# Kernel tuning notes

Measured on AMD Instinct MI355X. Metric: run time of the kernel, lower is better.

The kernel has to match this reference:

```python
import jax, jax.numpy as jnp
import numpy as np

B, L, D_MODEL = 8, 256, 256
D_STATE, D_INNER, DT_RANK, D_CONV = 16, 512, 16, 4


def _ln(x, g, b, eps):
    mu = x.mean(-1, keepdims=True)
    var = ((x - mu) ** 2).mean(-1, keepdims=True)
    return (x - mu) * jax.lax.rsqrt(var + eps) * g + b


def _ssm(x, W_in, conv_w, conv_b, W_x, W_dt, b_dt, A_log, Dp, W_out):
    # x: (B, L, D_MODEL) -- standard Mamba selective-scan block
    xz = x @ W_in                                  # (B,L,2*Di)
    xc, z = jnp.split(xz, 2, axis=-1)
    K = conv_w.shape[-1]
    xp = jnp.pad(xc, ((0, 0), (K - 1, 0), (0, 0)))  # causal depthwise conv
    xc = sum(xp[:, k:k + L, :] * conv_w[:, k] for k in range(K)) + conv_b
    xc = jax.nn.silu(xc)
    x_dbl = xc @ W_x                               # (B,L,R+2S)
    dt, Bm, Cm = jnp.split(x_dbl, [DT_RANK, DT_RANK + D_STATE], axis=-1)
    dt = jax.nn.softplus(dt @ W_dt + b_dt)         # (B,L,Di)
    A = -jnp.exp(A_log)                            # (Di,S)
    dA = jnp.exp(dt[..., None] * A)                # (B,L,Di,S)
    dBx = dt[..., None] * Bm[:, :, None, :] * xc[..., None]

    def step(h, inp):
        dA_t, dBx_t, C_t = inp
        h = dA_t * h + dBx_t                       # (B,Di,S)
        y = jnp.einsum('bds,bs->bd', h, C_t)
        return h, y

    h0 = jnp.zeros((xc.shape[0], D_INNER, D_STATE), xc.dtype)
    xs = (dA.transpose(1, 0, 2, 3), dBx.transpose(1, 0, 2, 3), Cm.transpose(1, 0, 2))
    _, ys = jax.lax.scan(step, h0, xs)             # (L,B,Di)
    y = ys.transpose(1, 0, 2) + xc * Dp
    y = y * jax.nn.silu(z)
    return y @ W_out


def _basic(x, ln_g, ln_b, ssm_params):
    # Basic_Block: ReLU(SSM(LN(x))) + x  (drop_path=0, attn_drop=0)
    return jax.nn.relu(_ssm(_ln(x, ln_g, ln_b, 1e-6), *ssm_params)) + x


def setup_inputs() -> dict:
    key = jax.random.key(0)
    ks = jax.random.split(key, 32)

    def n(k, shape, s=0.02):
        return jax.random.normal(k, shape, dtype=jnp.float32) * s

    inp = {}
    inp['x_spa'] = jax.random.normal(ks[0], (B, L, D_MODEL), dtype=jnp.float32)
    inp['x_spe'] = jax.random.normal(ks[1], (B, L, D_MODEL), dtype=jnp.float32)
    i = 2
    A_init = jnp.log(jnp.tile(jnp.arange(1, D_STATE + 1, dtype=jnp.float32), (D_INNER, 1)))
    for p in ('spa', 'spe'):
        inp[p + '_ln_g'] = jnp.ones((D_MODEL,), jnp.float32)
        inp[p + '_ln_b'] = jnp.zeros((D_MODEL,), jnp.float32)
        inp[p + '_W_in'] = n(ks[i], (D_MODEL, 2 * D_INNER)); i += 1
        inp[p + '_conv_w'] = n(ks[i], (D_INNER, D_CONV), 0.1); i += 1
        inp[p + '_conv_b'] = jnp.zeros((D_INNER,), jnp.float32)
        inp[p + '_W_x'] = n(ks[i], (D_INNER, DT_RANK + 2 * D_STATE)); i += 1
        inp[p + '_W_dt'] = n(ks[i], (DT_RANK, D_INNER), 0.1); i += 1
        inp[p + '_b_dt'] = n(ks[i], (D_INNER,), 0.1); i += 1
        inp[p + '_A_log'] = A_init
        inp[p + '_D'] = jnp.ones((D_INNER,), jnp.float32)
        inp[p + '_W_out'] = n(ks[i], (D_INNER, D_MODEL)); i += 1
    inp['sc_W'] = n(ks[i], (D_MODEL, D_MODEL)); i += 1
    inp['sc_b'] = jnp.zeros((D_MODEL,), jnp.float32)
    inp['sc_ln_g'] = jnp.ones((D_MODEL,), jnp.float32)
    inp['sc_ln_b'] = jnp.zeros((D_MODEL,), jnp.float32)
    inp['fusion_W'] = n(ks[i], (D_MODEL, D_MODEL))
    return inp


def reference(x_spa, x_spe,
              spa_ln_g, spa_ln_b, spa_W_in, spa_conv_w, spa_conv_b, spa_W_x,
              spa_W_dt, spa_b_dt, spa_A_log, spa_D, spa_W_out,
              spe_ln_g, spe_ln_b, spe_W_in, spe_conv_w, spe_conv_b, spe_W_x,
              spe_W_dt, spe_b_dt, spe_A_log, spe_D, spe_W_out,
              sc_W, sc_b, sc_ln_g, sc_ln_b, fusion_W):
    # shared shortcut: Linear + LayerNorm (eps=1e-5)
    ident_spa = _ln(x_spa @ sc_W + sc_b, sc_ln_g, sc_ln_b, 1e-5)
    ident_spe = _ln(x_spe @ sc_W + sc_b, sc_ln_g, sc_ln_b, 1e-5)
    spa_p = (spa_W_in, spa_conv_w, spa_conv_b, spa_W_x, spa_W_dt, spa_b_dt, spa_A_log, spa_D, spa_W_out)
    spe_p = (spe_W_in, spe_conv_w, spe_conv_b, spe_W_x, spe_W_dt, spe_b_dt, spe_A_log, spe_D, spe_W_out)
    a = _basic(x_spa, spa_ln_g, spa_ln_b, spa_p)
    e = _basic(x_spe, spe_ln_g, spe_ln_b, spe_p)
    # fusion gate: mean-pool both branches, Linear(no bias) + sigmoid, broadcast-mul
    fw = jax.nn.sigmoid(((a.mean(1) + e.mean(1)) * 0.5) @ fusion_W)[:, None, :]
    a = a * fw
    e = e * fw
    return (a + ident_spa, e + ident_spe)
```

## Files before the change

### kernel.cpp

```cpp
#include <hip/hip_runtime.h>
#include <hip/hip_bf16.h>
#include <math.h>

#define BD 8
#define LD 256
#define DM 256
#define DS 16
#define DI 512
#define RK 16

#define NROWS (2*BD*LD)
#define HALF_ROWS (BD*LD)

typedef __attribute__((ext_vector_type(8))) short bhalf8;
typedef __attribute__((ext_vector_type(4))) float f32x4;

__device__ __forceinline__ float siluf(float x){ return x / (1.f + __expf(-x)); }
__device__ __forceinline__ float softplusf(float x){
  return fmaxf(x, 0.f) + log1pf(__expf(-fabsf(x)));
}
__device__ __forceinline__ unsigned short f2bf(float f){
  __hip_bfloat16 h = __float2bfloat16(f);
  return *reinterpret_cast<unsigned short*>(&h);
}

__global__ __launch_bounds__(256) void k_prep(
    const float* __restrict__ Wi_spa, const float* __restrict__ Wi_spe,
    const float* __restrict__ Wo_spa, const float* __restrict__ Wo_spe,
    const float* __restrict__ scW,
    const float* __restrict__ Wx_spa, const float* __restrict__ Wx_spe,
    const float* __restrict__ x_spa, const float* __restrict__ x_spe,
    const float* __restrict__ g_spa, const float* __restrict__ b_spa,
    const float* __restrict__ g_spe, const float* __restrict__ b_spe,
    unsigned short* __restrict__ Wt_i_spa, unsigned short* __restrict__ Wt_i_spe,
    unsigned short* __restrict__ Wt_o_spa, unsigned short* __restrict__ Wt_o_spe,
    unsigned short* __restrict__ scWt,
    unsigned short* __restrict__ Wxt_spa, unsigned short* __restrict__ Wxt_spe,
    unsigned short* __restrict__ xnbf, unsigned short* __restrict__ xbf,
    float* __restrict__ pooled)
{
  __shared__ __align__(16) unsigned char smem[59904];
  int b = blockIdx.x;
  int tid = threadIdx.x;
  if (b == 60){
    for (int i=tid; i<BD*DM; i+=256) pooled[i] = 0.f;
    return;
  }
  if (b >= 61){
    float (*xst)[260] = (float (*)[260])smem;
    float (*red)[16]  = (float (*)[16])(smem + 16640);
    float *mu = (float*)(smem + 17664);
    float *rs = (float*)(smem + 17728);
    int r0g = (b - 61) * 16;
    int branch = r0g >= HALF_ROWS;
    const float* xb = branch ? x_spe : x_spa;
    const float* g  = branch ? g_spe : g_spa;
    const float* be = branch ? b_spe : b_spa;
    int rr0 = branch ? r0g - HALF_ROWS : r0g;
    for (int p=0;p<4;p++){
      int i4 = tid + 256*p;
      int r = i4 >> 6, c4 = (i4 & 63)*4;
      *(float4*)&xst[r][c4] = *(const float4*)(xb + (rr0+r)*DM + c4);
    }
    __syncthreads();
    {
      int row = tid >> 4, seg = tid & 15;
      float s = 0.f, s2 = 0.f;
      #pragma unroll
      for (int i=0;i<4;i++){
        float4 v = *(float4*)&xst[row][seg*16 + i*4];
        s  += v.x+v.y+v.z+v.w;
        s2 += v.x*v.x + v.y*v.y + v.z*v.z + v.w*v.w;
      }
      red[row][seg] = s;
      __syncthreads();
      if (seg == 0){
        float t=0.f;
        #pragma unroll
        for (int i=0;i<16;i++) t += red[row][i];
        mu[row] = t * (1.f/DM);
      }
      __syncthreads();
      red[row][seg] = s2;
      __syncthreads();
      if (seg == 0){
        float t=0.f;
        #pragma unroll
        for (int i=0;i<16;i++) t += red[row][i];
        float m = mu[row];
        rs[row] = rsqrtf(t*(1.f/DM) - m*m + 1e-6f);
      }
    }
    __syncthreads();
    for (int p=0;p<4;p++){
      int i4 = tid + 256*p;
      int r = i4 >> 6, c4 = (i4 & 63)*4;
      float4 v  = *(float4*)&xst[r][c4];
      float4 gv = *(const float4*)(g + c4);
      float4 bv = *(const float4*)(be + c4);
      float m = mu[r], rv = rs[r];
      unsigned int rlo = (unsigned int)f2bf(v.x) | ((unsigned int)f2bf(v.y) << 16);
      unsigned int rhi = (unsigned int)f2bf(v.z) | ((unsigned int)f2bf(v.w) << 16);
      *(uint2*)&xbf[(r0g+r)*DM + c4] = make_uint2(rlo, rhi);
      unsigned int nlo = (unsigned int)f2bf((v.x-m)*rv*gv.x + bv.x)
                       | ((unsigned int)f2bf((v.y-m)*rv*gv.y + bv.y) << 16);
      unsigned int nhi = (unsigned int)f2bf((v.z-m)*rv*gv.z + bv.z)
                       | ((unsigned int)f2bf((v.w-m)*rv*gv.w + bv.w) << 16);
      *(uint2*)&xnbf[(r0g+r)*DM + c4] = make_uint2(nlo, nhi);
    }
    return;
  }
  if (b >= 52){
    int bb = b - 52;
    int branch = bb >> 2, chunk = bb & 3;
    int k0 = chunk*128;
    const float* Wx = branch ? Wx_spe : Wx_spa;
    unsigned short* Wxt = branch ? Wxt_spe : Wxt_spa;
    float (*tile2)[49] = (float (*)[49])(smem + 34816);
    for (int i=tid; i<128*48; i+=256){
      int kk = i/48, c = i - kk*48;
      tile2[kk][c] = Wx[(k0+kk)*48 + c];
    }
    __syncthreads();
    for (int i=tid; i<64*128; i+=256){
      int cc = i >> 7, kk = i & 127;
      float v = (cc < 48) ? tile2[kk][cc] : 0.f;
      Wxt[cc*512 + k0 + kk] = f2bf(v);
    }
    return;
  }
  unsigned short (*tile)[68] = (unsigned short (*)[68])smem;
  const float* W; unsigned short* Wt; int N, K, c0, k0;
  if (b < 32){
    int bb = b & 15;
    W  = (b < 16) ? Wi_spa  : Wi_spe;
    Wt = (b < 16) ? Wt_i_spa: Wt_i_spe;
    N = 1024; K = 256; c0 = (bb >> 2)*256; k0 = (bb & 3)*64;
  } else if (b < 48){
    int bb = b - 32; int h = bb >> 3; bb &= 7;
    W  = h ? Wo_spe  : Wo_spa;
    Wt = h ? Wt_o_spe: Wt_o_spa;
    N = 256; K = 512; c0 = 0; k0 = bb*64;
  } else {
    int bb = b - 48;
    W = scW; Wt = scWt;
    N = 256; K = 256; c0 = 0; k0 = bb*64;
  }
  int c = c0 + tid;
  #pragma unroll 8
  for (int kk=0; kk<64; kk++)
    tile[tid][kk] = f2bf(W[(k0+kk)*N + c]);
  __syncthreads();
  for (int p=0; p<16; p++){
    int i = tid + 256*p;
    int cl = i >> 4, kq = (i & 15)*4;
    uint2 v = *(const uint2*)&tile[cl][kq];
    *(uint2*)&Wt[(c0+cl)*K + k0 + kq] = v;
  }
}

__global__ __launch_bounds__(256) void k_lnwin(
    const unsigned short* __restrict__ xnbf,
    const unsigned short* __restrict__ Wt_spa, const unsigned short* __restrict__ Wt_spe,
    float* __restrict__ xc_raw, float* __restrict__ szout)
{
  __shared__ unsigned short At[16][264];
  int tid = threadIdx.x;
  int bi = blockIdx.x;
  int rg = bi >> 2, cg = bi & 3;
  int r0 = rg * 16;
  int branch = (r0 >= HALF_ROWS);
  const unsigned short* Wt = branch ? Wt_spe : Wt_spa;
  for (int p=0;p<2;p++){
    int i = tid + 256*p;
    int r = i >> 5, oct = (i & 31)*8;
    *(uint4*)&At[r][oct] = *(const uint4*)&xnbf[(r0+r)*DM + oct];
  }
  __syncthreads();
  int w = tid >> 6, lane = tid & 63;
  int m16 = lane & 15, quad = lane >> 4;
  bhalf8 af[8];
  #pragma unroll
  for (int ks=0; ks<8; ks++)
    af[ks] = *(const bhalf8*)&At[m16][ks*32 + quad*8];
  f32x4 acc[4];
  #pragma unroll
  for (int ct=0; ct<4; ct++) acc[ct] = (f32x4)(0.f);
  const unsigned short* Wbw = Wt + (cg*256 + w*64)*256;
  #pragma unroll
  for (int ks=0; ks<8; ks++){
    #pragma unroll
    for (int ct=0; ct<4; ct++){
      bhalf8 bf = *(const bhalf8*)&Wbw[(ct*16 + m16)*256 + ks*32 + quad*8];
      acc[ct] = __builtin_amdgcn_mfma_f32_16x16x32_bf16(af[ks], bf, acc[ct], 0,0,0);
    }
  }
  bool isz = (cg >= 2);
  float* outp = isz ? szout : xc_raw;
  int cbase = (cg & 1)*256 + w*64;
  #pragma unroll
  for (int ct=0; ct<4; ct++){
    #pragma unroll
    for (int e=0;e<4;e++){
      int row = r0 + quad*4 + e;
      int col = cbase + ct*16 + m16;
      float v = acc[ct][e];
      if (isz) v = siluf(v);
      outp[row*DI + col] = v;
    }
  }
}

__global__ __launch_bounds__(256) void k_shortcut(
    const unsigned short* __restrict__ xbf,
    const unsigned short* __restrict__ scWt, const float* __restrict__ sc_b,
    const float* __restrict__ ln_g, const float* __restrict__ ln_b,
    float* __restrict__ ident)
{
  __shared__ unsigned short At[16][264];
  __shared__ float Dt[16][260];
  __shared__ float red[16][16];
  __shared__ float mu[16], rs[16];
  int tid = threadIdx.x;
  int r0 = blockIdx.x * 16;
  for (int p=0;p<2;p++){
    int i = tid + 256*p;
    int r = i >> 5, oct = (i & 31)*8;
    *(uint4*)&At[r][oct] = *(const uint4*)&xbf[(r0+r)*DM + oct];
  }
  __syncthreads();
  int w = tid >> 6, lane = tid & 63;
  int m16 = lane & 15, quad = lane >> 4;
  bhalf8 af[8];
  #pragma unroll
  for (int ks=0; ks<8; ks++)
    af[ks] = *(const bhalf8*)&At[m16][ks*32 + quad*8];
  f32x4 acc[4];
  #pragma unroll
  for (int ct=0; ct<4; ct++) acc[ct] = (f32x4)(0.f);
  const unsigned short* Wbw = scWt + (w*64)*256;
  #pragma unroll
  for (int ks=0; ks<8; ks++){
    #pragma unroll
    for (int ct=0; ct<4; ct++){
      bhalf8 bf = *(const bhalf8*)&Wbw[(ct*16 + m16)*256 + ks*32 + quad*8];
      acc[ct] = __builtin_amdgcn_mfma_f32_16x16x32_bf16(af[ks], bf, acc[ct], 0,0,0);
    }
  }
  #pragma unroll
  for (int ct=0; ct<4; ct++){
    #pragma unroll
    for (int e=0;e<4;e++){
      int row = quad*4 + e;
      int col = w*64 + ct*16 + m16;
      Dt[row][col] = acc[ct][e] + sc_b[col];
    }
  }
  __syncthreads();
  {
    int row = tid >> 4, seg = tid & 15;
    float s = 0.f, s2 = 0.f;
    #pragma unroll
    for (int i=0;i<4;i++){
      float4 v = *(const float4*)&Dt[row][seg*16 + i*4];
      s  += v.x+v.y+v.z+v.w;
      s2 += v.x*v.x + v.y*v.y + v.z*v.z + v.w*v.w;
    }
    red[row][seg] = s;
    __syncthreads();
    if (seg == 0){
      float t=0.f;
      #pragma unroll
      for (int i=0;i<16;i++) t += red[row][i];
      mu[row] = t * (1.f/DM);
    }
    __syncthreads();
    red[row][seg] = s2;
    __syncthreads();
    if (seg == 0){
      float t=0.f;
      #pragma unroll
      for (int i=0;i<16;i++) t += red[row][i];
      float m = mu[row];
      rs[row] = rsqrtf(t*(1.f/DM) - m*m + 1e-5f);
    }
  }
  __syncthreads();
  float gg = ln_g[tid], bb = ln_b[tid];
  #pragma unroll
  for (int r=0;r<16;r++)
    ident[(r0+r)*DM + tid] = (Dt[r][tid]-mu[r])*rs[r]*gg + bb;
}

__global__ __launch_bounds__(256) void k_convdbl(
    const float* __restrict__ cw_spa, const float* __restrict__ cb_spa,
    const float* __restrict__ cw_spe, const float* __restrict__ cb_spe,
    const float* __restrict__ xc_raw,
    const unsigned short* __restrict__ Wxt_spa, const unsigned short* __restrict__ Wxt_spe,
    const float* __restrict__ Wdt_spa, const float* __restrict__ bdt_spa,
    const float* __restrict__ Wdt_spe, const float* __restrict__ bdt_spe,
    float* __restrict__ xc, float* __restrict__ dt,
    float* __restrict__ Bm, float* __restrict__ Cm)
{
  __shared__ unsigned short At[16][520];
  __shared__ float xdbl[16][18];
  int tid = threadIdx.x;
  int r0 = blockIdx.x * 16;
  int branch = r0 >= HALF_ROWS;
  int l0 = r0 & (LD-1);
  const float* cw = branch ? cw_spe : cw_spa;
  const float* cb = branch ? cb_spe : cb_spa;
  const unsigned short* Wxt = branch ? Wxt_spe : Wxt_spa;
  const float* Wdt = branch ? Wdt_spe : Wdt_spa;
  const float* bdt = branch ? bdt_spe : bdt_spa;
  {
    int c = tid*2;
    float4 w0 = *(const float4*)(cw + 4*c);
    float4 w1 = *(const float4*)(cw + 4*(c+1));
    float2 bias = *(const float2*)(cb + c);
    float2 h0, h1, h2;
    if (l0 > 0){
      h0 = *(const float2*)(xc_raw + (r0-3)*DI + c);
      h1 = *(const float2*)(xc_raw + (r0-2)*DI + c);
      h2 = *(const float2*)(xc_raw + (r0-1)*DI + c);
    } else {
      h0 = make_float2(0.f,0.f); h1 = h0; h2 = h0;
    }
    #pragma unroll
    for (int r=0;r<16;r++){
      float2 cur = *(const float2*)(xc_raw + (r0+r)*DI + c);
      float vx = bias.x;
      vx = fmaf(h0.x, w0.x, vx); vx = fmaf(h1.x, w0.y, vx);
      vx = fmaf(h2.x, w0.z, vx); vx = fmaf(cur.x, w0.w, vx);
      float vy = bias.y;
      vy = fmaf(h0.y, w1.x, vy); vy = fmaf(h1.y, w1.y, vy);
      vy = fmaf(h2.y, w1.z, vy); vy = fmaf(cur.y, w1.w, vy);
      vx = siluf(vx); vy = siluf(vy);
      *(float2*)(xc + (r0+r)*DI + c) = make_float2(vx, vy);
      unsigned int pk = (unsigned int)f2bf(vx) | ((unsigned int)f2bf(vy) << 16);
      *(unsigned int*)&At[r][c] = pk;
      h0 = h1; h1 = h2; h2 = cur;
    }
  }
  __syncthreads();
  int w = tid >> 6, lane = tid & 63;
  int m16 = lane & 15, quad = lane >> 4;
  f32x4 acc = (f32x4)(0.f);
  #pragma unroll
  for (int ks=0; ks<16; ks++){
    bhalf8 a = *(const bhalf8*)&At[m16][ks*32 + quad*8];
    bhalf8 bf = *(const bhalf8*)&Wxt[(w*16 + m16)*512 + ks*32 + quad*8];
    acc = __builtin_amdgcn_mfma_f32_16x16x32_bf16(a, bf, acc, 0,0,0);
  }
  #pragma unroll
  for (int e=0;e<4;e++){
    int row = quad*4 + e;
    float v = acc[e];
    if (w == 0)      xdbl[row][m16] = v;
    else if (w == 1) Bm[(r0+row)*DS + m16] = v;
    else if (w == 2) Cm[(r0+row)*DS + m16] = v;
  }
  __syncthreads();
  float wdt0[16], wdt1[16];
  #pragma unroll
  for (int j=0;j<16;j++){ wdt0[j]=Wdt[j*DI+tid]; wdt1[j]=Wdt[j*DI+tid+256]; }
  float b0 = bdt[tid], b1 = bdt[tid+256];
  #pragma unroll
  for (int r=0;r<16;r++){
    float a0=b0, a1=b1;
    #pragma unroll
    for (int j=0;j<16;j++){
      float xv = xdbl[r][j];
      a0 = fmaf(xv, wdt0[j], a0);
      a1 = fmaf(xv, wdt1[j], a1);
    }
    dt[(r0+r)*DI + tid]       = softplusf(a0);
    dt[(r0+r)*DI + tid + 256] = softplusf(a1);
  }
}

__global__ __launch_bounds__(256) void k_scan(
    const float* __restrict__ Alog_spa, const float* __restrict__ Dp_spa,
    const float* __restrict__ Alog_spe, const float* __restrict__ Dp_spe,
    const float* __restrict__ dt, const float* __restrict__ xc,
    const float* __restrict__ sz, const float* __restrict__ Bm,
    const float* __restrict__ Cm, unsigned short* __restrict__ ybf)
{
  __shared__ float dts[16][20], xcs[16][20];
  __shared__ float ypbuf[16][260];
  __shared__ float Dsh[16];
  int tid = threadIdx.x;
  int bi = blockIdx.x;
  int branch = bi >> 8;
  int rem = bi & 255;
  int b = rem >> 5;
  int d0 = (rem & 31) * 16;
  const float* Alog = branch ? Alog_spe : Alog_spa;
  const float* Dp   = branch ? Dp_spe   : Dp_spa;
  int dg = tid >> 4, s = tid & 15;
  int d = d0 + dg;
  float A_ds = -__expf(Alog[d*DS + s]);
  if (tid < 16) Dsh[tid] = Dp[d0 + tid];
  int row0 = branch*HALF_ROWS + b*LD;
  float h = 0.f;
  for (int c=0; c<16; c++){
    int rbase = row0 + c*16;
    float rB[16], rC[16];
    #pragma unroll
    for (int li=0; li<16; li++){
      rB[li] = Bm[(rbase+li)*DS + s];
      rC[li] = Cm[(rbase+li)*DS + s];
    }
    if (tid < 128){
      int arr = tid >> 6, j = tid & 63;
      int r = j >> 2, c4 = (j & 3)*4;
      if (arr == 0) *(float4*)&dts[r][c4] = *(const float4*)(dt + (rbase+r)*DI + d0 + c4);
      else          *(float4*)&xcs[r][c4] = *(const float4*)(xc + (rbase+r)*DI + d0 + c4);
    }
    __syncthreads();
    float rdt[16], rxc[16];
    #pragma unroll
    for (int li=0; li<16; li++){ rdt[li] = dts[li][dg]; rxc[li] = xcs[li][dg]; }
    float yp[16];
    #pragma unroll
    for (int li=0; li<16; li++){
      float dA = __expf(rdt[li] * A_ds);
      h = fmaf(dA, h, rdt[li] * rB[li] * rxc[li]);
      yp[li] = h * rC[li];
    }
    #pragma unroll
    for (int li=0; li<16; li++)
      ypbuf[li][s*16 + ((dg + s) & 15)] = yp[li];
    __syncthreads();
    float acc = 0.f;
    #pragma unroll
    for (int ss=0; ss<16; ss++)
      acc += ypbuf[dg][ss*16 + ((s + ss) & 15)];
    float xcv = xc[(rbase+dg)*DI + d0 + s];
    float szv = sz[(rbase+dg)*DI + d0 + s];
    float yv = fmaf(xcv, Dsh[s], acc) * szv;
    ybf[(rbase+dg)*DI + d0 + s] = f2bf(yv);
    __syncthreads();
  }
}

__global__ __launch_bounds__(256) void k_wout(
    const unsigned short* __restrict__ Wt_spa, const unsigned short* __restrict__ Wt_spe,
    const float* __restrict__ x_spa, const float* __restrict__ x_spe,
    const unsigned short* __restrict__ ybf, float* __restrict__ ae,
    float* __restrict__ pooled)
{
  __shared__ unsigned short At[16][520];
  int tid = threadIdx.x;
  int bi = blockIdx.x;
  int r0 = (bi >> 1) * 16;
  int ch = bi & 1;
  int branch = (r0 >= HALF_ROWS);
  const unsigned short* Wt = branch ? Wt_spe : Wt_spa;
  const float* xb = branch ? x_spe : x_spa;
  int rr0 = branch ? r0 - HALF_ROWS : r0;
  for (int p=0;p<4;p++){
    int i = tid + 256*p;
    int r = i >> 6, oct = (i & 63)*8;
    *(uint4*)&At[r][oct] = *(const uint4*)&ybf[(r0+r)*DI + oct];
  }
  __syncthreads();
  int w = tid >> 6, lane = tid & 63;
  int m16 = lane & 15, quad = lane >> 4;
  bhalf8 af[16];
  #pragma unroll
  for (int ks=0; ks<16; ks++)
    af[ks] = *(const bhalf8*)&At[m16][ks*32 + quad*8];
  f32x4 acc[2];
  #pragma unroll
  for (int ct=0; ct<2; ct++) acc[ct] = (f32x4)(0.f);
  const unsigned short* Wbw = Wt + (ch*128 + w*32)*512;
  #pragma unroll
  for (int ks=0; ks<16; ks++){
    #pragma unroll
    for (int ct=0; ct<2; ct++){
      bhalf8 bf = *(const bhalf8*)&Wbw[(ct*16 + m16)*512 + ks*32 + quad*8];
      acc[ct] = __builtin_amdgcn_mfma_f32_16x16x32_bf16(af[ks], bf, acc[ct], 0,0,0);
    }
  }
  float ps0 = 0.f, ps1 = 0.f;
  #pragma unroll
  for (int ct=0; ct<2; ct++){
    #pragma unroll
    for (int e=0;e<4;e++){
      int row = quad*4 + e;
      int col = ch*128 + w*32 + ct*16 + m16;
      float v = fmaxf(acc[ct][e], 0.f) + xb[(rr0+row)*DM + col];
      ae[(r0+row)*DM + col] = v;
      if (ct == 0) ps0 += v; else ps1 += v;
    }
  }
  ps0 += __shfl_xor(ps0, 16, 64); ps0 += __shfl_xor(ps0, 32, 64);
  ps1 += __shfl_xor(ps1, 16, 64); ps1 += __shfl_xor(ps1, 32, 64);
  if (quad == 0){
    int bidx = (r0 >> 8) & 7;
    atomicAdd(&pooled[bidx*DM + ch*128 + w*32 + m16],      ps0);
    atomicAdd(&pooled[bidx*DM + ch*128 + w*32 + 16 + m16], ps1);
  }
}

__global__ __launch_bounds__(256) void k_gate(const float* __restrict__ pooled,
    const float* __restrict__ fW, float* __restrict__ fw)
{
  __shared__ float p[DM];
  int b=blockIdx.x, c=threadIdx.x;
  p[c] = pooled[b*DM+c] * (0.5f/LD);
  __syncthreads();
  float a=0.f;
  for(int k=0;k<DM;k+=4){
    a = fmaf(p[k+0], fW[(k+0)*DM+c], a);
    a = fmaf(p[k+1], fW[(k+1)*DM+c], a);
    a = fmaf(p[k+2], fW[(k+2)*DM+c], a);
    a = fmaf(p[k+3], fW[(k+3)*DM+c], a);
  }
  fw[b*DM+c]=1.f/(1.f+__expf(-a));
}

__global__ __launch_bounds__(256) void k_final(const float* __restrict__ ae,
    const float* __restrict__ ident, const float* __restrict__ fw, float* __restrict__ out)
{
  int idx4 = blockIdx.x*256 + threadIdx.x;
  int row = idx4 >> 6;
  int b = (row >> 8) & 7;
  int c4 = (idx4 & 63) * 4;
  float4 av = *(const float4*)(ae + idx4*4);
  float4 iv = *(const float4*)(ident + idx4*4);
  float4 fv = *(const float4*)(fw + b*DM + c4);
  float4 o;
  o.x = fmaf(av.x, fv.x, iv.x);
  o.y = fmaf(av.y, fv.y, iv.y);
  o.z = fmaf(av.z, fv.z, iv.z);
  o.w = fmaf(av.w, fv.w, iv.w);
  *(float4*)(out + idx4*4) = o;
}

extern "C" void kernel_launch(void* const* d_in, const int* in_sizes, int n_in,
                              void* d_out, int out_size, void* d_ws, size_t ws_size,
                              hipStream_t stream) {
  const float* x_spa     = (const float*)d_in[0];
  const float* x_spe     = (const float*)d_in[1];
  const float* spa_ln_g  = (const float*)d_in[2];
  const float* spa_ln_b  = (const float*)d_in[3];
  const float* spa_W_in  = (const float*)d_in[4];
  const float* spa_cw    = (const float*)d_in[5];
  const float* spa_cb    = (const float*)d_in[6];
  const float* spa_W_x   = (const float*)d_in[7];
  const float* spa_W_dt  = (const float*)d_in[8];
  const float* spa_b_dt  = (const float*)d_in[9];
  const float* spa_A_log = (const float*)d_in[10];
  const float* spa_D     = (const float*)d_in[11];
  const float* spa_W_out = (const float*)d_in[12];
  const float* spe_ln_g  = (const float*)d_in[13];
  const float* spe_ln_b  = (const float*)d_in[14];
  const float* spe_W_in  = (const float*)d_in[15];
  const float* spe_cw    = (const float*)d_in[16];
  const float* spe_cb    = (const float*)d_in[17];
  const float* spe_W_x   = (const float*)d_in[18];
  const float* spe_W_dt  = (const float*)d_in[19];
  const float* spe_b_dt  = (const float*)d_in[20];
  const float* spe_A_log = (const float*)d_in[21];
  const float* spe_D     = (const float*)d_in[22];
  const float* spe_W_out = (const float*)d_in[23];
  const float* sc_W      = (const float*)d_in[24];
  const float* sc_b      = (const float*)d_in[25];
  const float* sc_ln_g   = (const float*)d_in[26];
  const float* sc_ln_b   = (const float*)d_in[27];
  const float* fusion_W  = (const float*)d_in[28];

  float* ws = (float*)d_ws;
  float* ident  = ws;
  float* xc_raw = ident  + NROWS*DM;
  float* sz     = xc_raw + NROWS*DI;
  float* xc     = sz     + NROWS*DI;
  float* dt     = xc     + NROWS*DI;
  float* Bm     = dt     + NROWS*DI;
  float* Cm     = Bm     + NROWS*DS;
  float* pooled = Cm     + NROWS*DS;
  float* fw     = pooled + BD*DM;
  unsigned short* Wt_i_spa = (unsigned short*)(fw + BD*DM);
  unsigned short* Wt_i_spe = Wt_i_spa + 1024*256;
  unsigned short* Wt_o_spa = Wt_i_spe + 1024*256;
  unsigned short* Wt_o_spe = Wt_o_spa + 256*512;
  unsigned short* scWt     = Wt_o_spe + 256*512;
  unsigned short* Wxt_spa  = scWt     + 256*256;
  unsigned short* Wxt_spe  = Wxt_spa  + 64*512;
  unsigned short* xnbf     = Wxt_spe  + 64*512;
  unsigned short* xbf      = xnbf     + NROWS*DM;

  float* out = (float*)d_out;

  k_prep<<<317, 256, 0, stream>>>(spa_W_in, spe_W_in, spa_W_out, spe_W_out, sc_W,
                                  spa_W_x, spe_W_x, x_spa, x_spe,
                                  spa_ln_g, spa_ln_b, spe_ln_g, spe_ln_b,
                                  Wt_i_spa, Wt_i_spe, Wt_o_spa, Wt_o_spe, scWt,
                                  Wxt_spa, Wxt_spe, xnbf, xbf, pooled);
  k_lnwin<<<1024, 256, 0, stream>>>(xnbf, Wt_i_spa, Wt_i_spe, xc_raw, sz);
  k_convdbl<<<NROWS/16, 256, 0, stream>>>(spa_cw, spa_cb, spe_cw, spe_cb, xc_raw,
                                          Wxt_spa, Wxt_spe,
                                          spa_W_dt, spa_b_dt, spe_W_dt, spe_b_dt,
                                          xc, dt, Bm, Cm);
  unsigned short* ybf = (unsigned short*)xc_raw;
  k_scan<<<512, 256, 0, stream>>>(spa_A_log, spa_D, spe_A_log, spe_D, dt, xc, sz, Bm, Cm, ybf);
  k_shortcut<<<NROWS/16, 256, 0, stream>>>(xbf, scWt, sc_b, sc_ln_g, sc_ln_b, ident);
  float* ae = dt;
  k_wout<<<512, 256, 0, stream>>>(Wt_o_spa, Wt_o_spe, x_spa, x_spe, ybf, ae, pooled);
  k_gate<<<BD, 256, 0, stream>>>(pooled, fusion_W, fw);
  k_final<<<NROWS*DM/1024, 256, 0, stream>>>(ae, ident, fw, out);
}
```

Baseline: 210.4 us.

## Pre-swizzle weights into MFMA fragment order, merge shortcut GEMM, restage scan chunks

Result: no change. 208.9 us (-0.7%).

```diff
diff --git a/kernel.cpp b/kernel.cpp
--- a/kernel.cpp
+++ b/kernel.cpp
@@ -23,6 +23,7 @@
   __hip_bfloat16 h = __float2bfloat16(f);
   return *reinterpret_cast<unsigned short*>(&h);
 }
+
 
 __global__ __launch_bounds__(256) void k_prep(
     const float* __restrict__ Wi_spa, const float* __restrict__ Wi_spe,
@@ -125,7 +126,10 @@
     for (int i=tid; i<64*128; i+=256){
       int cc = i >> 7, kk = i & 127;
       float v = (cc < 48) ? tile2[kk][cc] : 0.f;
-      Wxt[cc*512 + k0 + kk] = f2bf(v);
+      int kg = k0 + kk;
+      int ct = cc >> 4, m16 = cc & 15;
+      int ks = kg >> 5, quad = (kg >> 3) & 3, j = kg & 7;
+      Wxt[((ct*16 + ks)*64 + quad*16 + m16)*8 + j] = f2bf(v);
     }
     return;
   }
@@ -151,145 +155,143 @@
   for (int kk=0; kk<64; kk++)
     tile[tid][kk] = f2bf(W[(k0+kk)*N + c]);
   __syncthreads();
+  int ksegs = K >> 5;
   for (int p=0; p<16; p++){
     int i = tid + 256*p;
     int cl = i >> 4, kq = (i & 15)*4;
+    int cg = c0 + cl;
+    int ct = cg >> 4, m16 = cg & 15;
+    int kg = k0 + kq;
+    int ks = kg >> 5, quad = (kg >> 3) & 3, j = kg & 7;
     uint2 v = *(const uint2*)&tile[cl][kq];
-    *(uint2*)&Wt[(c0+cl)*K + k0 + kq] = v;
-  }
-}
-
-__global__ __launch_bounds__(256) void k_lnwin(
-    const unsigned short* __restrict__ xnbf,
+    *(uint2*)&Wt[((ct*ksegs + ks)*64 + quad*16 + m16)*8 + j] = v;
+  }
+}
+
+__global__ __launch_bounds__(256) void k_gemm1(
+    const unsigned short* __restrict__ xnbf, const unsigned short* __restrict__ xbf,
     const unsigned short* __restrict__ Wt_spa, const unsigned short* __restrict__ Wt_spe,
-    float* __restrict__ xc_raw, float* __restrict__ szout)
-{
-  __shared__ unsigned short At[16][264];
-  int tid = threadIdx.x;
-  int bi = blockIdx.x;
-  int rg = bi >> 2, cg = bi & 3;
-  int r0 = rg * 16;
-  int branch = (r0 >= HALF_ROWS);
-  const unsigned short* Wt = branch ? Wt_spe : Wt_spa;
-  for (int p=0;p<2;p++){
-    int i = tid + 256*p;
-    int r = i >> 5, oct = (i & 31)*8;
-    *(uint4*)&At[r][oct] = *(const uint4*)&xnbf[(r0+r)*DM + oct];
-  }
-  __syncthreads();
-  int w = tid >> 6, lane = tid & 63;
-  int m16 = lane & 15, quad = lane >> 4;
-  bhalf8 af[8];
-  #pragma unroll
-  for (int ks=0; ks<8; ks++)
-    af[ks] = *(const bhalf8*)&At[m16][ks*32 + quad*8];
-  f32x4 acc[4];
-  #pragma unroll
-  for (int ct=0; ct<4; ct++) acc[ct] = (f32x4)(0.f);
-  const unsigned short* Wbw = Wt + (cg*256 + w*64)*256;
-  #pragma unroll
-  for (int ks=0; ks<8; ks++){
-    #pragma unroll
-    for (int ct=0; ct<4; ct++){
-      bhalf8 bf = *(const bhalf8*)&Wbw[(ct*16 + m16)*256 + ks*32 + quad*8];
-      acc[ct] = __builtin_amdgcn_mfma_f32_16x16x32_bf16(af[ks], bf, acc[ct], 0,0,0);
-    }
-  }
-  bool isz = (cg >= 2);
-  float* outp = isz ? szout : xc_raw;
-  int cbase = (cg & 1)*256 + w*64;
-  #pragma unroll
-  for (int ct=0; ct<4; ct++){
-    #pragma unroll
-    for (int e=0;e<4;e++){
-      int row = r0 + quad*4 + e;
-      int col = cbase + ct*16 + m16;
-      float v = acc[ct][e];
-      if (isz) v = siluf(v);
-      outp[row*DI + col] = v;
-    }
-  }
-}
-
-__global__ __launch_bounds__(256) void k_shortcut(
-    const unsigned short* __restrict__ xbf,
     const unsigned short* __restrict__ scWt, const float* __restrict__ sc_b,
     const float* __restrict__ ln_g, const float* __restrict__ ln_b,
-    float* __restrict__ ident)
+    float* __restrict__ xc_raw, float* __restrict__ szout, float* __restrict__ ident)
 {
   __shared__ unsigned short At[16][264];
   __shared__ float Dt[16][260];
   __shared__ float red[16][16];
   __shared__ float mu[16], rs[16];
   int tid = threadIdx.x;
-  int r0 = blockIdx.x * 16;
-  for (int p=0;p<2;p++){
-    int i = tid + 256*p;
-    int r = i >> 5, oct = (i & 31)*8;
-    *(uint4*)&At[r][oct] = *(const uint4*)&xbf[(r0+r)*DM + oct];
-  }
-  __syncthreads();
+  int bi = blockIdx.x;
   int w = tid >> 6, lane = tid & 63;
   int m16 = lane & 15, quad = lane >> 4;
-  bhalf8 af[8];
-  #pragma unroll
-  for (int ks=0; ks<8; ks++)
-    af[ks] = *(const bhalf8*)&At[m16][ks*32 + quad*8];
-  f32x4 acc[4];
-  #pragma unroll
-  for (int ct=0; ct<4; ct++) acc[ct] = (f32x4)(0.f);
-  const unsigned short* Wbw = scWt + (w*64)*256;
-  #pragma unroll
-  for (int ks=0; ks<8; ks++){
+  if (bi < 1024){
+    int rg = bi >> 2, cg = bi & 3;
+    int r0 = rg * 16;
+    int branch = (r0 >= HALF_ROWS);
+    const unsigned short* Wt = branch ? Wt_spe : Wt_spa;
+    for (int p=0;p<2;p++){
+      int i = tid + 256*p;
+      int r = i >> 5, oct = (i & 31)*8;
+      *(uint4*)&At[r][oct] = *(const uint4*)&xnbf[(r0+r)*DM + oct];
+    }
+    __syncthreads();
+    bhalf8 af[8];
+    #pragma unroll
+    for (int ks=0; ks<8; ks++)
+      af[ks] = *(const bhalf8*)&At[m16][ks*32 + quad*8];
+    f32x4 acc[4];
+    #pragma unroll
+    for (int ct=0; ct<4; ct++) acc[ct] = (f32x4)(0.f);
+    #pragma unroll
+    for (int ks=0; ks<8; ks++){
+      #pragma unroll
+      for (int ct=0; ct<4; ct++){
+        int f = (cg*16 + w*4 + ct)*8 + ks;
+        bhalf8 bf = *(const bhalf8*)&Wt[f*512 + lane*8];
+        acc[ct] = __builtin_amdgcn_mfma_f32_16x16x32_bf16(af[ks], bf, acc[ct], 0,0,0);
+      }
+    }
+    bool isz = (cg >= 2);
+    float* outp = isz ? szout : xc_raw;
+    int cbase = (cg & 1)*256 + w*64;
     #pragma unroll
     for (int ct=0; ct<4; ct++){
-      bhalf8 bf = *(const bhalf8*)&Wbw[(ct*16 + m16)*256 + ks*32 + quad*8];
-      acc[ct] = __builtin_amdgcn_mfma_f32_16x16x32_bf16(af[ks], bf, acc[ct], 0,0,0);
-    }
-  }
-  #pragma unroll
-  for (int ct=0; ct<4; ct++){
-    #pragma unroll
-    for (int e=0;e<4;e++){
-      int row = quad*4 + e;
-      int col = w*64 + ct*16 + m16;
-      Dt[row][col] = acc[ct][e] + sc_b[col];
-    }
-  }
-  __syncthreads();
-  {
-    int row = tid >> 4, seg = tid & 15;
-    float s = 0.f, s2 = 0.f;
-    #pragma unroll
-    for (int i=0;i<4;i++){
-      float4 v = *(const float4*)&Dt[row][seg*16 + i*4];
-      s  += v.x+v.y+v.z+v.w;
-      s2 += v.x*v.x + v.y*v.y + v.z*v.z + v.w*v.w;
-    }
-    red[row][seg] = s;
-    __syncthreads();
-    if (seg == 0){
-      float t=0.f;
       #pragma unroll
-      for (int i=0;i<16;i++) t += red[row][i];
-      mu[row] = t * (1.f/DM);
-    }
-    __syncthreads();
-    red[row][seg] = s2;
-    __syncthreads();
-    if (seg == 0){
-      float t=0.f;
+      for (int e=0;e<4;e++){
+        int row = r0 + quad*4 + e;
+        int col = cbase + ct*16 + m16;
+        float v = acc[ct][e];
+        if (isz) v = siluf(v);
+        outp[row*DI + col] = v;
+      }
+    }
+  } else {
+    int r0 = (bi - 1024) * 16;
+    for (int p=0;p<2;p++){
+      int i = tid + 256*p;
+      int r = i >> 5, oct = (i & 31)*8;
+      *(uint4*)&At[r][oct] = *(const uint4*)&xbf[(r0+r)*DM + oct];
+    }
+    __syncthreads();
+    bhalf8 af[8];
+    #pragma unroll
+    for (int ks=0; ks<8; ks++)
+      af[ks] = *(const bhalf8*)&At[m16][ks*32 + quad*8];
+    f32x4 acc[4];
+    #pragma unroll
+    for (int ct=0; ct<4; ct++) acc[ct] = (f32x4)(0.f);
+    #pragma unroll
+    for (int ks=0; ks<8; ks++){
       #pragma unroll
-      for (int i=0;i<16;i++) t += red[row][i];
-      float m = mu[row];
-      rs[row] = rsqrtf(t*(1.f/DM) - m*m + 1e-5f);
-    }
-  }
-  __syncthreads();
-  float gg = ln_g[tid], bb = ln_b[tid];
-  #pragma unroll
-  for (int r=0;r<16;r++)
-    ident[(r0+r)*DM + tid] = (Dt[r][tid]-mu[r])*rs[r]*gg + bb;
+      for (int ct=0; ct<4; ct++){
+        int f = (w*4 + ct)*8 + ks;
+        bhalf8 bf = *(const bhalf8*)&scWt[f*512 + lane*8];
+        acc[ct] = __builtin_amdgcn_mfma_f32_16x16x32_bf16(af[ks], bf, acc[ct], 0,0,0);
+      }
+    }
+    #pragma unroll
+    for (int ct=0; ct<4; ct++){
+      #pragma unroll
+      for (int e=0;e<4;e++){
+        int row = quad*4 + e;
+        int col = w*64 + ct*16 + m16;
+        Dt[row][col] = acc[ct][e] + sc_b[col];
+      }
+    }
+    __syncthreads();
+    {
+      int row = tid >> 4, seg = tid & 15;
+      float s = 0.f, s2 = 0.f;
+      #pragma unroll
+      for (int i=0;i<4;i++){
+        float4 v = *(const float4*)&Dt[row][seg*16 + i*4];
+        s  += v.x+v.y+v.z+v.w;
+        s2 += v.x*v.x + v.y*v.y + v.z*v.z + v.w*v.w;
+      }
+      red[row][seg] = s;
+      __syncthreads();
+      if (seg == 0){
+        float t=0.f;
+        #pragma unroll
+        for (int i=0;i<16;i++) t += red[row][i];
+        mu[row] = t * (1.f/DM);
+      }
+      __syncthreads();
+      red[row][seg] = s2;
+      __syncthreads();
+      if (seg == 0){
+        float t=0.f;
+        #pragma unroll
+        for (int i=0;i<16;i++) t += red[row][i];
+        float m = mu[row];
+        rs[row] = rsqrtf(t*(1.f/DM) - m*m + 1e-5f);
+      }
+    }
+    __syncthreads();
+    float gg = ln_g[tid], bb = ln_b[tid];
+    #pragma unroll
+    for (int r=0;r<16;r++)
+      ident[(r0+r)*DM + tid] = (Dt[r][tid]-mu[r])*rs[r]*gg + bb;
+  }
 }
 
 __global__ __launch_bounds__(256) void k_convdbl(
@@ -349,7 +351,8 @@
   #pragma unroll
   for (int ks=0; ks<16; ks++){
     bhalf8 a = *(const bhalf8*)&At[m16][ks*32 + quad*8];
-    bhalf8 bf = *(const bhalf8*)&Wxt[(w*16 + m16)*512 + ks*32 + quad*8];
+    int f = w*16 + ks;
+    bhalf8 bf = *(const bhalf8*)&Wxt[f*512 + lane*8];
     acc = __builtin_amdgcn_mfma_f32_16x16x32_bf16(a, bf, acc, 0,0,0);
   }
   #pragma unroll
@@ -386,8 +389,7 @@
     const float* __restrict__ sz, const float* __restrict__ Bm,
     const float* __restrict__ Cm, unsigned short* __restrict__ ybf)
 {
-  __shared__ float dts[16][20], xcs[16][20];
-  __shared__ float ypbuf[16][260];
+  __shared__ float dts[32][20], xcs[32][20], szs[32][20], Bs[32][20], Cs[32][20];
   __shared__ float Dsh[16];
   int tid = threadIdx.x;
   int bi = blockIdx.x;
@@ -403,43 +405,48 @@
   if (tid < 16) Dsh[tid] = Dp[d0 + tid];
   int row0 = branch*HALF_ROWS + b*LD;
   float h = 0.f;
-  for (int c=0; c<16; c++){
-    int rbase = row0 + c*16;
-    float rB[16], rC[16];
-    #pragma unroll
-    for (int li=0; li<16; li++){
-      rB[li] = Bm[(rbase+li)*DS + s];
-      rC[li] = Cm[(rbase+li)*DS + s];
-    }
-    if (tid < 128){
-      int arr = tid >> 6, j = tid & 63;
+  for (int c=0; c<8; c++){
+    int rbase = row0 + c*32;
+    for (int idx=tid; idx<640; idx+=256){
+      int arr = idx >> 7;
+      int j = idx & 127;
       int r = j >> 2, c4 = (j & 3)*4;
-      if (arr == 0) *(float4*)&dts[r][c4] = *(const float4*)(dt + (rbase+r)*DI + d0 + c4);
-      else          *(float4*)&xcs[r][c4] = *(const float4*)(xc + (rbase+r)*DI + d0 + c4);
-    }
-    __syncthreads();
-    float rdt[16], rxc[16];
-    #pragma unroll
-    for (int li=0; li<16; li++){ rdt[li] = dts[li][dg]; rxc[li] = xcs[li][dg]; }
-    float yp[16];
-    #pragma unroll
-    for (int li=0; li<16; li++){
-      float dA = __expf(rdt[li] * A_ds);
-      h = fmaf(dA, h, rdt[li] * rB[li] * rxc[li]);
-      yp[li] = h * rC[li];
-    }
-    #pragma unroll
-    for (int li=0; li<16; li++)
-      ypbuf[li][s*16 + ((dg + s) & 15)] = yp[li];
-    __syncthreads();
-    float acc = 0.f;
-    #pragma unroll
-    for (int ss=0; ss<16; ss++)
-      acc += ypbuf[dg][ss*16 + ((s + ss) & 15)];
-    float xcv = xc[(rbase+dg)*DI + d0 + s];
-    float szv = sz[(rbase+dg)*DI + d0 + s];
-    float yv = fmaf(xcv, Dsh[s], acc) * szv;
-    ybf[(rbase+dg)*DI + d0 + s] = f2bf(yv);
+      float4 v;
+      if      (arr == 0) v = *(const float4*)(dt + (rbase+r)*DI + d0 + c4);
+      else if (arr == 1) v = *(const float4*)(xc + (rbase+r)*DI + d0 + c4);
+      else if (arr == 2) v = *(const float4*)(sz + (rbase+r)*DI + d0 + c4);
+      else if (arr == 3) v = *(const float4*)(Bm + (rbase+r)*DS + c4);
+      else               v = *(const float4*)(Cm + (rbase+r)*DS + c4);
+      if      (arr == 0) *(float4*)&dts[r][c4] = v;
+      else if (arr == 1) *(float4*)&xcs[r][c4] = v;
+      else if (arr == 2) *(float4*)&szs[r][c4] = v;
+      else if (arr == 3) *(float4*)&Bs[r][c4]  = v;
+      else               *(float4*)&Cs[r][c4]  = v;
+    }
+    __syncthreads();
+    float yp[32];
+    #pragma unroll
+    for (int li=0; li<32; li++){
+      float dtv = dts[li][dg];
+      float xcv = xcs[li][dg];
+      float dA = __expf(dtv * A_ds);
+      h = fmaf(dA, h, dtv * Bs[li][s] * xcv);
+      yp[li] = h * Cs[li][s];
+    }
+    #pragma unroll
+    for (int li=0; li<32; li++){
+      yp[li] += __shfl_xor(yp[li], 1, 64);
+      yp[li] += __shfl_xor(yp[li], 2, 64);
+      yp[li] += __shfl_xor(yp[li], 4, 64);
+      yp[li] += __shfl_xor(yp[li], 8, 64);
+    }
+    {
+      float Dv = Dsh[dg];
+      float v0 = fmaf(xcs[s][dg],    Dv, yp[s])    * szs[s][dg];
+      float v1 = fmaf(xcs[s+16][dg], Dv, yp[s+16]) * szs[s+16][dg];
+      ybf[(rbase+s)*DI    + d0 + dg] = f2bf(v0);
+      ybf[(rbase+s+16)*DI + d0 + dg] = f2bf(v1);
+    }
     __syncthreads();
   }
 }
@@ -474,12 +481,12 @@
   f32x4 acc[2];
   #pragma unroll
   for (int ct=0; ct<2; ct++) acc[ct] = (f32x4)(0.f);
-  const unsigned short* Wbw = Wt + (ch*128 + w*32)*512;
   #pragma unroll
   for (int ks=0; ks<16; ks++){
     #pragma unroll
     for (int ct=0; ct<2; ct++){
-      bhalf8 bf = *(const bhalf8*)&Wbw[(ct*16 + m16)*512 + ks*32 + quad*8];
+      int f = (ch*8 + w*2 + ct)*16 + ks;
+      bhalf8 bf = *(const bhalf8*)&Wt[f*512 + lane*8];
       acc[ct] = __builtin_amdgcn_mfma_f32_16x16x32_bf16(af[ks], bf, acc[ct], 0,0,0);
     }
   }
@@ -599,14 +606,14 @@
                                   spa_ln_g, spa_ln_b, spe_ln_g, spe_ln_b,
                                   Wt_i_spa, Wt_i_spe, Wt_o_spa, Wt_o_spe, scWt,
                                   Wxt_spa, Wxt_spe, xnbf, xbf, pooled);
-  k_lnwin<<<1024, 256, 0, stream>>>(xnbf, Wt_i_spa, Wt_i_spe, xc_raw, sz);
+  k_gemm1<<<1280, 256, 0, stream>>>(xnbf, xbf, Wt_i_spa, Wt_i_spe, scWt, sc_b,
+                                    sc_ln_g, sc_ln_b, xc_raw, sz, ident);
   k_convdbl<<<NROWS/16, 256, 0, stream>>>(spa_cw, spa_cb, spe_cw, spe_cb, xc_raw,
                                           Wxt_spa, Wxt_spe,
                                           spa_W_dt, spa_b_dt, spe_W_dt, spe_b_dt,
                                           xc, dt, Bm, Cm);
   unsigned short* ybf = (unsigned short*)xc_raw;
   k_scan<<<512, 256, 0, stream>>>(spa_A_log, spa_D, spe_A_log, spe_D, dt, xc, sz, Bm, Cm, ybf);
-  k_shortcut<<<NROWS/16, 256, 0, stream>>>(xbf, scWt, sc_b, sc_ln_g, sc_ln_b, ident);
   float* ae = dt;
   k_wout<<<512, 256, 0, stream>>>(Wt_o_spa, Wt_o_spe, x_spa, x_spe, ybf, ae, pooled);
   k_gate<<<BD, 256, 0, stream>>>(pooled, fusion_W, fw);
```
